# Optimization experiments

Hardware: AMD Instinct MI355X
Metric: run time of the kernel (lower is better)

## Reference

```python
import jax, jax.numpy as jnp
import numpy as np

N_HEAD = 16

def setup_inputs() -> dict:
    key = jax.random.key(0)
    k1, k2, k3 = jax.random.split(key, 3)
    B, T, C = 4, 2048, 1024
    x = jax.random.normal(k1, (B, T, C), dtype=jnp.float32)
    W_qkv = jax.random.normal(k2, (3 * C, C), dtype=jnp.float32) * 0.02
    W_o = jax.random.normal(k3, (C, C), dtype=jnp.float32) * (0.02 / np.sqrt(2.0))
    return {"x": x, "W_qkv": W_qkv, "W_o": W_o}

def reference(x, W_qkv, W_o):
    B, T, C = x.shape
    H = N_HEAD
    d_k = C // H
    # combined qkv projection (torch Linear: y = x @ W^T)
    qkv = x @ W_qkv.T                      # (B, T, 3C)
    q, k, v = jnp.split(qkv, 3, axis=-1)
    def split_heads(t):
        return t.reshape(B, T, H, d_k).transpose(0, 2, 1, 3)  # (B, H, T, d_k)
    q, k, v = split_heads(q), split_heads(k), split_heads(v)
    scale = 1.0 / jnp.sqrt(jnp.asarray(d_k, dtype=x.dtype))
    scores = jnp.einsum('bhqd,bhkd->bhqk', q, k) * scale      # (B, H, T, T)
    causal = jnp.tril(jnp.ones((T, T), dtype=bool))           # True = keep
    scores = jnp.where(causal[None, None], scores, -jnp.inf)
    attn = jax.nn.softmax(scores, axis=-1)                    # no NaNs under causal mask
    out = jnp.einsum('bhqk,bhkd->bhqd', attn, v)              # (B, H, T, d_k)
    out = out.transpose(0, 2, 1, 3).reshape(B, T, C)
    return out @ W_o.T
```

## Files before the change

kernel.cpp:

```cpp
#include <hip/hip_runtime.h>
#include <hip/hip_bf16.h>
#include <cstdint>

typedef __bf16 bf16;
typedef __bf16 bf16x8 __attribute__((ext_vector_type(8)));
typedef float f32x4 __attribute__((ext_vector_type(4)));

#define MFMA16(A, B, C) __builtin_amdgcn_mfma_f32_16x16x32_bf16((A), (B), (C), 0, 0, 0)

__device__ __forceinline__ void async16(const bf16* g, bf16* l) {
    __builtin_amdgcn_global_load_lds(
        (const __attribute__((address_space(1))) void*)g,
        (__attribute__((address_space(3))) void*)l, 16, 0, 0);
}

__global__ void cvt_bf16(const float* __restrict__ src, bf16* __restrict__ dst) {
    const size_t i = (size_t)(blockIdx.x * 256 + threadIdx.x) * 8;
    const float4 a = *(const float4*)(src + i);
    const float4 b = *(const float4*)(src + i + 4);
    bf16x8 r;
    r[0] = (bf16)a.x; r[1] = (bf16)a.y; r[2] = (bf16)a.z; r[3] = (bf16)a.w;
    r[4] = (bf16)b.x; r[5] = (bf16)b.y; r[6] = (bf16)b.z; r[7] = (bf16)b.w;
    *(bf16x8*)(dst + i) = r;
}

template <int MODE>
__launch_bounds__(256, 3)
__global__ void gemm_nt(const bf16* __restrict__ A, const bf16* __restrict__ Bm,
                        void* __restrict__ O0, bf16* __restrict__ O1,
                        bf16* __restrict__ O2, int N, int K) {
    __shared__ alignas(16) bf16 As[128 * 64];
    __shared__ alignas(16) bf16 Bs[128 * 64];

    const int t = threadIdx.x;
    const int w = t >> 6, l = t & 63, quad = l >> 4, l15 = l & 15;
    const int wm = w & 1, wn = w >> 1;
    const int m0 = blockIdx.y * 128, n0 = blockIdx.x * 128;

    f32x4 acc[4][4] = {};

    const int srow = t >> 3, sch = t & 7;
    const bf16* ga = A + (size_t)(m0 + srow) * K + sch * 8;
    const bf16* gb = Bm + (size_t)(n0 + srow) * K + sch * 8;

    for (int kt = 0; kt < K; kt += 64) {
        __syncthreads();
#pragma unroll
        for (int i = 0; i < 4; i++) {
            async16(ga + (size_t)i * 32 * K + kt, &As[(i * 256 + t) * 8]);
            async16(gb + (size_t)i * 32 * K + kt, &Bs[(i * 256 + t) * 8]);
        }
        __syncthreads();

#pragma unroll
        for (int s = 0; s < 2; s++) {
            bf16x8 af[4], bfr[4];
#pragma unroll
            for (int im = 0; im < 4; im++)
                af[im] = *(const bf16x8*)&As[(wm * 64 + im * 16 + l15) * 64 + s * 32 + quad * 8];
#pragma unroll
            for (int in = 0; in < 4; in++)
                bfr[in] = *(const bf16x8*)&Bs[(wn * 64 + in * 16 + l15) * 64 + s * 32 + quad * 8];
#pragma unroll
            for (int im = 0; im < 4; im++)
#pragma unroll
                for (int in = 0; in < 4; in++)
                    acc[im][in] = MFMA16(af[im], bfr[in], acc[im][in]);
        }
    }

    if (MODE == 0) {
        bf16* Q0 = (bf16*)O0;
#pragma unroll
        for (int in = 0; in < 4; in++) {
            const int n = n0 + wn * 64 + in * 16;
            const int sel = n >> 10;
            const int c = n & 1023;
            const int h = c >> 6;
            const int dd = c & 63;
            bf16* dst = (sel == 0) ? Q0 : ((sel == 1) ? O1 : O2);
#pragma unroll
            for (int im = 0; im < 4; im++) {
#pragma unroll
                for (int r = 0; r < 4; r++) {
                    const int m = m0 + wm * 64 + im * 16 + quad * 4 + r;
                    const int b = m >> 11, tt = m & 2047;
                    dst[((size_t)(b * 16 + h) * 2048 + tt) * 64 + dd + l15] =
                        (bf16)acc[im][in][r];
                }
            }
        }
    } else {
        float* Of = (float*)O0;
#pragma unroll
        for (int im = 0; im < 4; im++) {
#pragma unroll
            for (int in = 0; in < 4; in++) {
#pragma unroll
                for (int r = 0; r < 4; r++) {
                    const int m = m0 + wm * 64 + im * 16 + quad * 4 + r;
                    const int n = n0 + wn * 64 + in * 16 + l15;
                    Of[(size_t)m * N + n] = acc[im][in][r];
                }
            }
        }
    }
}

__launch_bounds__(256, 4)
__global__ void vtrans(const bf16* __restrict__ V, bf16* __restrict__ Vt) {
    __shared__ alignas(16) bf16 Ls[64 * 72];
    const int t = threadIdx.x, bh = blockIdx.y, tt = blockIdx.x;
#pragma unroll
    for (int i = 0; i < 2; i++) {
        const int id = i * 256 + t, r = id >> 3, c = id & 7;
        *(bf16x8*)&Ls[r * 72 + c * 8] =
            *(const bf16x8*)&V[((size_t)bh * 2048 + tt * 64 + r) * 64 + c * 8];
    }
    __syncthreads();
#pragma unroll
    for (int i = 0; i < 2; i++) {
        const int id = i * 256 + t, d = id >> 3, c = id & 7;
        bf16x8 v;
#pragma unroll
        for (int j = 0; j < 8; j++) v[j] = Ls[(c * 8 + j) * 72 + d];
        *(bf16x8*)&Vt[((size_t)bh * 64 + d) * 2048 + tt * 64 + c * 8] = v;
    }
}

__launch_bounds__(256, 4)
__global__ void attn_fwd(const bf16* __restrict__ Q, const bf16* __restrict__ Kk,
                         const bf16* __restrict__ Vt, bf16* __restrict__ O) {
    __shared__ alignas(16) bf16 Ks[64 * 72];
    __shared__ alignas(16) bf16 Vs[64 * 72];
    __shared__ alignas(16) bf16 Ps[4][16 * 72];

    const int t = threadIdx.x, w = t >> 6, l = t & 63;
    const int quad = l >> 4, l15 = l & 15;
    const int bh = blockIdx.y, pair = blockIdx.x;
    const int b = bh >> 4, h = bh & 15;
    const int sr = t >> 3, sc = t & 7;

    const float M2 = 43.2808512f;
    const bf16* Kbase = Kk + (size_t)bh * 2048 * 64;
    const bf16* Vbase = Vt + (size_t)bh * 64 * 2048;

#pragma unroll
    for (int half = 0; half < 2; half++) {
        const int qt = half ? (31 - pair) : pair;

        const int qrow = qt * 64 + w * 16 + l15;
        bf16x8 aq0 = *(const bf16x8*)&Q[((size_t)bh * 2048 + qrow) * 64 + quad * 8];
        bf16x8 aq1 = *(const bf16x8*)&Q[((size_t)bh * 2048 + qrow) * 64 + 32 + quad * 8];
#pragma unroll
        for (int j = 0; j < 8; j++) {
            aq0[j] = aq0[j] * (bf16)0.1803369f;
            aq1[j] = aq1[j] * (bf16)0.1803369f;
        }

        float li[4] = {0.f, 0.f, 0.f, 0.f};
        f32x4 oa[4] = {};

        for (int kt = 0; kt <= qt; kt++) {
            bf16x8 rk0 = *(const bf16x8*)&Kbase[(size_t)(kt * 64 + sr) * 64 + sc * 8];
            bf16x8 rk1 = *(const bf16x8*)&Kbase[(size_t)(kt * 64 + sr + 32) * 64 + sc * 8];
            bf16x8 rv0 = *(const bf16x8*)&Vbase[(size_t)sr * 2048 + kt * 64 + sc * 8];
            bf16x8 rv1 = *(const bf16x8*)&Vbase[(size_t)(sr + 32) * 2048 + kt * 64 + sc * 8];
            __syncthreads();
            *(bf16x8*)&Ks[sr * 72 + sc * 8] = rk0;
            *(bf16x8*)&Ks[(sr + 32) * 72 + sc * 8] = rk1;
            *(bf16x8*)&Vs[sr * 72 + sc * 8] = rv0;
            *(bf16x8*)&Vs[(sr + 32) * 72 + sc * 8] = rv1;
            __syncthreads();

            const bool diag = (kt == qt);
#pragma unroll
            for (int nt = 0; nt < 4; nt++) {
                bf16x8 b0 = *(const bf16x8*)&Ks[(nt * 16 + l15) * 72 + quad * 8];
                bf16x8 b1 = *(const bf16x8*)&Ks[(nt * 16 + l15) * 72 + 32 + quad * 8];
                f32x4 s = {};
                s = MFMA16(aq0, b0, s);
                s = MFMA16(aq1, b1, s);
                const int colg = nt * 16 + l15;
#pragma unroll
                for (int r = 0; r < 4; r++) {
                    float sv = s[r];
                    if (diag && colg > (w * 16 + quad * 4 + r)) sv = -1e30f;
                    const float p = exp2f(sv - M2);
                    li[r] += p;
                    Ps[w][(quad * 4 + r) * 72 + nt * 16 + l15] = (bf16)p;
                }
            }

#pragma unroll
            for (int s = 0; s < 2; s++) {
                bf16x8 ap = *(const bf16x8*)&Ps[w][l15 * 72 + s * 32 + quad * 8];
#pragma unroll
                for (int nt = 0; nt < 4; nt++) {
                    bf16x8 bv = *(const bf16x8*)&Vs[(nt * 16 + l15) * 72 + s * 32 + quad * 8];
                    oa[nt] = MFMA16(ap, bv, oa[nt]);
                }
            }
        }

#pragma unroll
        for (int r = 0; r < 4; r++) {
            li[r] += __shfl_xor(li[r], 1);
            li[r] += __shfl_xor(li[r], 2);
            li[r] += __shfl_xor(li[r], 4);
            li[r] += __shfl_xor(li[r], 8);
        }

#pragma unroll
        for (int nt = 0; nt < 4; nt++) {
#pragma unroll
            for (int r = 0; r < 4; r++) {
                const int m = b * 2048 + qt * 64 + w * 16 + quad * 4 + r;
                O[(size_t)m * 1024 + h * 64 + nt * 16 + l15] = (bf16)(oa[nt][r] / li[r]);
            }
        }
        __syncthreads();
    }
}

extern "C" void kernel_launch(void* const* d_in, const int* in_sizes, int n_in,
                              void* d_out, int out_size, void* d_ws, size_t ws_size,
                              hipStream_t stream) {
    const float* x = (const float*)d_in[0];
    const float* wqkv = (const float*)d_in[1];
    const float* wo = (const float*)d_in[2];

    const size_t SZ = (size_t)8192 * 1024;
    bf16* xb = (bf16*)d_ws;
    bf16* wqb = xb + SZ;
    bf16* wob = wqb + (size_t)3072 * 1024;
    bf16* Qw = wob + (size_t)1024 * 1024;
    bf16* Kw = Qw + SZ;
    bf16* Vw = Kw + SZ;
    bf16* Vtw = xb;

    dim3 blk(256);
    cvt_bf16<<<4096, blk, 0, stream>>>(x, xb);
    cvt_bf16<<<1536, blk, 0, stream>>>(wqkv, wqb);
    cvt_bf16<<<512, blk, 0, stream>>>(wo, wob);
    gemm_nt<0><<<dim3(24, 64), blk, 0, stream>>>(xb, wqb, Qw, Kw, Vw, 3072, 1024);
    vtrans<<<dim3(32, 64), blk, 0, stream>>>(Vw, Vtw);
    attn_fwd<<<dim3(16, 64), blk, 0, stream>>>(Qw, Kw, Vtw, Vw);
    gemm_nt<1><<<dim3(8, 64), blk, 0, stream>>>(Vw, wob, d_out, nullptr, nullptr, 1024, 1024);
}
```

Before: 283.3 us.

## Process 128 query rows per attention block, load K from global into registers

```diff
diff --git a/kernel.cpp b/kernel.cpp
--- a/kernel.cpp
+++ b/kernel.cpp
@@ -14,14 +14,23 @@
         (__attribute__((address_space(3))) void*)l, 16, 0, 0);
 }
 
-__global__ void cvt_bf16(const float* __restrict__ src, bf16* __restrict__ dst) {
-    const size_t i = (size_t)(blockIdx.x * 256 + threadIdx.x) * 8;
-    const float4 a = *(const float4*)(src + i);
-    const float4 b = *(const float4*)(src + i + 4);
+__global__ void cvt_all(const float* __restrict__ x, const float* __restrict__ wq,
+                        const float* __restrict__ wo, bf16* __restrict__ xb,
+                        bf16* __restrict__ wqb, bf16* __restrict__ wob) {
+    const int bid = blockIdx.x;
+    const float* s;
+    bf16* d;
+    int off;
+    if (bid < 4096)      { s = x;  d = xb;  off = bid; }
+    else if (bid < 5632) { s = wq; d = wqb; off = bid - 4096; }
+    else                 { s = wo; d = wob; off = bid - 5632; }
+    const size_t i = ((size_t)off * 256 + threadIdx.x) * 8;
+    const float4 a = *(const float4*)(s + i);
+    const float4 b2 = *(const float4*)(s + i + 4);
     bf16x8 r;
     r[0] = (bf16)a.x; r[1] = (bf16)a.y; r[2] = (bf16)a.z; r[3] = (bf16)a.w;
-    r[4] = (bf16)b.x; r[5] = (bf16)b.y; r[6] = (bf16)b.z; r[7] = (bf16)b.w;
-    *(bf16x8*)(dst + i) = r;
+    r[4] = (bf16)b2.x; r[5] = (bf16)b2.y; r[6] = (bf16)b2.z; r[7] = (bf16)b2.w;
+    *(bf16x8*)(d + i) = r;
 }
 
 template <int MODE>
@@ -128,12 +137,11 @@
     }
 }
 
-__launch_bounds__(256, 4)
+__launch_bounds__(256, 2)
 __global__ void attn_fwd(const bf16* __restrict__ Q, const bf16* __restrict__ Kk,
                          const bf16* __restrict__ Vt, bf16* __restrict__ O) {
-    __shared__ alignas(16) bf16 Ks[64 * 72];
     __shared__ alignas(16) bf16 Vs[64 * 72];
-    __shared__ alignas(16) bf16 Ps[4][16 * 72];
+    __shared__ alignas(16) bf16 Ps[4][32 * 72];
 
     const int t = threadIdx.x, w = t >> 6, l = t & 63;
     const int quad = l >> 4, l15 = l & 15;
@@ -142,84 +150,107 @@
     const int sr = t >> 3, sc = t & 7;
 
     const float M2 = 43.2808512f;
+    const bf16* Qbase = Q + (size_t)bh * 2048 * 64;
     const bf16* Kbase = Kk + (size_t)bh * 2048 * 64;
     const bf16* Vbase = Vt + (size_t)bh * 64 * 2048;
 
 #pragma unroll
     for (int half = 0; half < 2; half++) {
-        const int qt = half ? (31 - pair) : pair;
-
-        const int qrow = qt * 64 + w * 16 + l15;
-        bf16x8 aq0 = *(const bf16x8*)&Q[((size_t)bh * 2048 + qrow) * 64 + quad * 8];
-        bf16x8 aq1 = *(const bf16x8*)&Q[((size_t)bh * 2048 + qrow) * 64 + 32 + quad * 8];
-#pragma unroll
-        for (int j = 0; j < 8; j++) {
-            aq0[j] = aq0[j] * (bf16)0.1803369f;
-            aq1[j] = aq1[j] * (bf16)0.1803369f;
-        }
-
-        float li[4] = {0.f, 0.f, 0.f, 0.f};
-        f32x4 oa[4] = {};
-
-        for (int kt = 0; kt <= qt; kt++) {
-            bf16x8 rk0 = *(const bf16x8*)&Kbase[(size_t)(kt * 64 + sr) * 64 + sc * 8];
-            bf16x8 rk1 = *(const bf16x8*)&Kbase[(size_t)(kt * 64 + sr + 32) * 64 + sc * 8];
+        const int qt = half ? (15 - pair) : pair;
+
+        bf16x8 aq[2][2];
+#pragma unroll
+        for (int rg = 0; rg < 2; rg++) {
+            const int qrow = qt * 128 + rg * 64 + w * 16 + l15;
+            aq[rg][0] = *(const bf16x8*)&Qbase[(size_t)qrow * 64 + quad * 8];
+            aq[rg][1] = *(const bf16x8*)&Qbase[(size_t)qrow * 64 + 32 + quad * 8];
+#pragma unroll
+            for (int j = 0; j < 8; j++) {
+                aq[rg][0][j] = aq[rg][0][j] * (bf16)0.1803369f;
+                aq[rg][1][j] = aq[rg][1][j] * (bf16)0.1803369f;
+            }
+        }
+
+        float li[2][4] = {};
+        f32x4 oa[2][4] = {};
+        const int ktmax = 2 * qt + 1;
+
+        for (int kt = 0; kt <= ktmax; kt++) {
+            bf16x8 kb0[4], kb1[4];
+#pragma unroll
+            for (int nt = 0; nt < 4; nt++) {
+                const bf16* kp = &Kbase[(size_t)(kt * 64 + nt * 16 + l15) * 64 + quad * 8];
+                kb0[nt] = *(const bf16x8*)kp;
+                kb1[nt] = *(const bf16x8*)(kp + 32);
+            }
             bf16x8 rv0 = *(const bf16x8*)&Vbase[(size_t)sr * 2048 + kt * 64 + sc * 8];
             bf16x8 rv1 = *(const bf16x8*)&Vbase[(size_t)(sr + 32) * 2048 + kt * 64 + sc * 8];
             __syncthreads();
-            *(bf16x8*)&Ks[sr * 72 + sc * 8] = rk0;
-            *(bf16x8*)&Ks[(sr + 32) * 72 + sc * 8] = rk1;
             *(bf16x8*)&Vs[sr * 72 + sc * 8] = rv0;
             *(bf16x8*)&Vs[(sr + 32) * 72 + sc * 8] = rv1;
             __syncthreads();
 
-            const bool diag = (kt == qt);
+            const bool skip0 = (kt == ktmax);
+
+#pragma unroll
+            for (int rg = 0; rg < 2; rg++) {
+                if (rg == 0 && skip0) continue;
+                const bool diag = (kt == 2 * qt + rg);
+#pragma unroll
+                for (int nt = 0; nt < 4; nt++) {
+                    f32x4 s = {};
+                    s = MFMA16(aq[rg][0], kb0[nt], s);
+                    s = MFMA16(aq[rg][1], kb1[nt], s);
+                    const int colg = nt * 16 + l15;
+#pragma unroll
+                    for (int r = 0; r < 4; r++) {
+                        float sv = s[r];
+                        if (diag && colg > (w * 16 + quad * 4 + r)) sv = -1e30f;
+                        const float p = exp2f(sv - M2);
+                        li[rg][r] += p;
+                        Ps[w][(rg * 16 + quad * 4 + r) * 72 + nt * 16 + l15] = (bf16)p;
+                    }
+                }
+            }
+
+            bf16x8 bv[2][4];
+#pragma unroll
+            for (int s2 = 0; s2 < 2; s2++)
+#pragma unroll
+                for (int nt = 0; nt < 4; nt++)
+                    bv[s2][nt] = *(const bf16x8*)&Vs[(nt * 16 + l15) * 72 + s2 * 32 + quad * 8];
+#pragma unroll
+            for (int rg = 0; rg < 2; rg++) {
+                if (rg == 0 && skip0) continue;
+#pragma unroll
+                for (int s2 = 0; s2 < 2; s2++) {
+                    bf16x8 ap = *(const bf16x8*)&Ps[w][(rg * 16 + l15) * 72 + s2 * 32 + quad * 8];
+#pragma unroll
+                    for (int nt = 0; nt < 4; nt++)
+                        oa[rg][nt] = MFMA16(ap, bv[s2][nt], oa[rg][nt]);
+                }
+            }
+        }
+
+#pragma unroll
+        for (int rg = 0; rg < 2; rg++) {
+#pragma unroll
+            for (int r = 0; r < 4; r++) {
+                li[rg][r] += __shfl_xor(li[rg][r], 1);
+                li[rg][r] += __shfl_xor(li[rg][r], 2);
+                li[rg][r] += __shfl_xor(li[rg][r], 4);
+                li[rg][r] += __shfl_xor(li[rg][r], 8);
+            }
 #pragma unroll
             for (int nt = 0; nt < 4; nt++) {
-                bf16x8 b0 = *(const bf16x8*)&Ks[(nt * 16 + l15) * 72 + quad * 8];
-                bf16x8 b1 = *(const bf16x8*)&Ks[(nt * 16 + l15) * 72 + 32 + quad * 8];
-                f32x4 s = {};
-                s = MFMA16(aq0, b0, s);
-                s = MFMA16(aq1, b1, s);
-                const int colg = nt * 16 + l15;
 #pragma unroll
                 for (int r = 0; r < 4; r++) {
-                    float sv = s[r];
-                    if (diag && colg > (w * 16 + quad * 4 + r)) sv = -1e30f;
-                    const float p = exp2f(sv - M2);
-                    li[r] += p;
-                    Ps[w][(quad * 4 + r) * 72 + nt * 16 + l15] = (bf16)p;
-                }
-            }
-
-#pragma unroll
-            for (int s = 0; s < 2; s++) {
-                bf16x8 ap = *(const bf16x8*)&Ps[w][l15 * 72 + s * 32 + quad * 8];
-#pragma unroll
-                for (int nt = 0; nt < 4; nt++) {
-                    bf16x8 bv = *(const bf16x8*)&Vs[(nt * 16 + l15) * 72 + s * 32 + quad * 8];
-                    oa[nt] = MFMA16(ap, bv, oa[nt]);
-                }
-            }
-        }
-
-#pragma unroll
-        for (int r = 0; r < 4; r++) {
-            li[r] += __shfl_xor(li[r], 1);
-            li[r] += __shfl_xor(li[r], 2);
-            li[r] += __shfl_xor(li[r], 4);
-            li[r] += __shfl_xor(li[r], 8);
-        }
-
-#pragma unroll
-        for (int nt = 0; nt < 4; nt++) {
-#pragma unroll
-            for (int r = 0; r < 4; r++) {
-                const int m = b * 2048 + qt * 64 + w * 16 + quad * 4 + r;
-                O[(size_t)m * 1024 + h * 64 + nt * 16 + l15] = (bf16)(oa[nt][r] / li[r]);
-            }
-        }
-        __syncthreads();
+                    const int m = b * 2048 + qt * 128 + rg * 64 + w * 16 + quad * 4 + r;
+                    O[(size_t)m * 1024 + h * 64 + nt * 16 + l15] =
+                        (bf16)(oa[rg][nt][r] / li[rg][r]);
+                }
+            }
+        }
     }
 }
 
@@ -240,11 +271,9 @@
     bf16* Vtw = xb;
 
     dim3 blk(256);
-    cvt_bf16<<<4096, blk, 0, stream>>>(x, xb);
-    cvt_bf16<<<1536, blk, 0, stream>>>(wqkv, wqb);
-    cvt_bf16<<<512, blk, 0, stream>>>(wo, wob);
+    cvt_all<<<6144, blk, 0, stream>>>(x, wqkv, wo, xb, wqb, wob);
     gemm_nt<0><<<dim3(24, 64), blk, 0, stream>>>(xb, wqb, Qw, Kw, Vw, 3072, 1024);
     vtrans<<<dim3(32, 64), blk, 0, stream>>>(Vw, Vtw);
-    attn_fwd<<<dim3(16, 64), blk, 0, stream>>>(Qw, Kw, Vtw, Vw);
+    attn_fwd<<<dim3(8, 64), blk, 0, stream>>>(Qw, Kw, Vtw, Vw);
     gemm_nt<1><<<dim3(8, 64), blk, 0, stream>>>(Vw, wob, d_out, nullptr, nullptr, 1024, 1024);
 }
```

Result: no change. 286.7 us (+1.2%).
